# Optimization experiments

Measured on AMD Instinct MI355X. Metric: run time of the kernel, lower is better.

The kernel has to match this reference:

```python
import jax, jax.numpy as jnp
import numpy as np

B, H, S, DK = 4, 16, 2048, 128
NEG = -1e9  # large-negative stand-in for -inf additive mask
CAUSAL = True  # module constructed with mask=True (decoder self-attention)


def setup_inputs() -> dict:
    key = jax.random.key(0)
    kq, kk, kv, kl = jax.random.split(key, 4)
    q = jax.random.normal(kq, (B, H, S, DK), dtype=jnp.float32)
    k = jax.random.normal(kk, (B, H, S, DK), dtype=jnp.float32)
    v = jax.random.normal(kv, (B, H, S, DK), dtype=jnp.float32)
    sen_len = jax.random.randint(kl, (B,), 1, S + 1, dtype=jnp.int32)
    return {"q": q, "k": k, "v": v, "sen_len": sen_len}


def reference(q, k, v, sen_len):
    # att = q @ k^T / sqrt(d)   -> (B, H, S, S)
    scale = 1.0 / jnp.sqrt(jnp.asarray(DK, dtype=q.dtype))
    att = jnp.einsum('bhqd,bhkd->bhqk', q, k) * scale

    # Fused padding (+ optional causal) mask, multiplicative zero-mask and
    # additive -inf mask, exactly as att*zero_mask + inf_mask in the original.
    pos = jnp.arange(S)
    valid = pos[None, :] < sen_len[:, None]                 # (B, S) token validity
    zmask = (valid[:, :, None] & valid[:, None, :])         # (B, S, S) pad mask
    if CAUSAL:
        zmask = zmask & (pos[None, :, None] >= pos[None, None, :])
    zmask = zmask[:, None, :, :].astype(att.dtype)          # (B, 1, S, S)
    att = att * zmask + NEG * (1.0 - zmask)

    att = jax.nn.softmax(att, axis=-1)
    return jnp.einsum('bhqk,bhkd->bhqd', att, v)
```

## Files before the change

kernel.cpp:

```cpp
#include <hip/hip_runtime.h>
#include <hip/hip_bf16.h>

#define Bb   4
#define Hh   16
#define Ss   2048
#define Dd   128
#define QBLK 128
#define KVB  32

typedef __attribute__((ext_vector_type(8))) short bf16x8;
typedef __attribute__((ext_vector_type(4))) float f32x4;
typedef __attribute__((ext_vector_type(4))) float fvec4;
typedef __attribute__((ext_vector_type(2))) unsigned u32x2;
typedef __attribute__((ext_vector_type(4))) unsigned u32x4;

__device__ __forceinline__ unsigned pk2(float a, float b) {
    __hip_bfloat162 h = __float22bfloat162_rn(make_float2(a, b));
    unsigned u; __builtin_memcpy(&u, &h, 4); return u;
}

typedef const __attribute__((address_space(1))) char* gas_t;
typedef __attribute__((address_space(3))) char* las_t;
__device__ __forceinline__ void gld16(const void* g, void* l) {
    __builtin_amdgcn_global_load_lds((gas_t)g, (las_t)l, 16, 0, 0);
}

__global__ __launch_bounds__(256) void cvtkf_kernel(const float* __restrict__ K,
                                                    short* __restrict__ Kf) {
    const int bh = blockIdx.x >> 5, ch = blockIdx.x & 31;
    const int tid = threadIdx.x;
    const float* Kb = K + ((size_t)bh * Ss + ch * 64) * Dd;
    short* out = Kf + ((size_t)(bh * 64 + ch * 2)) * 4096;
    #pragma unroll
    for (int i = 0; i < 4; ++i) {
        int c = tid + 256 * i;
        int kt = c >> 9, r = c & 511;
        int mt = r >> 8, kc = (r >> 6) & 3, l = r & 63;
        int g = l >> 4, qc = l & 15;
        const fvec4* p = (const fvec4*)(Kb + (size_t)(kt * 32 + mt * 16 + qc) * Dd
                                        + kc * 32 + g * 8);
        fvec4 a = p[0], b = p[1];
        u32x4 u;
        u[0] = pk2(a[0], a[1]); u[1] = pk2(a[2], a[3]);
        u[2] = pk2(b[0], b[1]); u[3] = pk2(b[2], b[3]);
        *(u32x4*)(out + c * 8) = u;
    }
}

__global__ __launch_bounds__(256) void cvtvf_kernel(const float* __restrict__ V,
                                                    short* __restrict__ Vf,
                                                    float* __restrict__ part) {
    __shared__ float bins[128];
    const int bh = blockIdx.x >> 5, ch = blockIdx.x & 31;
    const int tid = threadIdx.x;
    if (tid < 128) bins[tid] = 0.f;
    __syncthreads();
    const float* Vb = V + ((size_t)bh * Ss + ch * 64) * Dd;
    short* out = Vf + ((size_t)(bh * 64 + ch * 2)) * 4096;
    #pragma unroll
    for (int i = 0; i < 4; ++i) {
        int c = tid + 256 * i;
        int kt = c >> 9, r = c & 511;
        int dt = r >> 6, l = r & 63;
        int g = l >> 4, qc = l & 15;
        int d = dt * 16 + qc;
        const float* src = Vb + (size_t)(kt * 32 + g * 8) * Dd + d;
        float v[8]; float s = 0.f;
        #pragma unroll
        for (int j = 0; j < 8; ++j) { v[j] = src[(size_t)j * Dd]; s += v[j]; }
        atomicAdd(&bins[d], s);
        u32x4 u;
        u[0] = pk2(v[0], v[1]); u[1] = pk2(v[2], v[3]);
        u[2] = pk2(v[4], v[5]); u[3] = pk2(v[6], v[7]);
        *(u32x4*)(out + c * 8) = u;
    }
    __syncthreads();
    if (tid < 128) part[(size_t)blockIdx.x * Dd + tid] = bins[tid];
}

__global__ __launch_bounds__(256) void vpart_kernel(const float* __restrict__ V,
                                                    float* __restrict__ part) {
    int blk = blockIdx.x, bh = blk >> 3, ch = blk & 7;
    int tid = threadIdx.x, d4 = tid & 31, rg = tid >> 5;
    const fvec4* p = (const fvec4*)(V + ((size_t)bh * Ss + ch * 256) * Dd) + d4;
    fvec4 s = {0.f, 0.f, 0.f, 0.f};
    for (int rr = 0; rr < 32; ++rr) s += p[(size_t)(rg * 32 + rr) * 32];
    __shared__ fvec4 red[256];
    red[tid] = s;
    __syncthreads();
    for (int off = 128; off >= 32; off >>= 1) {
        if (tid < off) red[tid] += red[tid + off];
        __syncthreads();
    }
    if (tid < 32) ((fvec4*)(part + (size_t)blk * Dd))[tid] = red[tid];
}

__global__ __launch_bounds__(128) void vcomb_kernel(const float* __restrict__ part,
                                                    float* __restrict__ vm, int nch) {
    int bh = blockIdx.x, d = threadIdx.x;
    float s = 0.f;
    for (int c = 0; c < nch; ++c) s += part[(size_t)(bh * nch + c) * Dd + d];
    vm[bh * Dd + d] = s * (1.0f / 2048.0f);
}

__global__ __launch_bounds__(256) void attn4_kernel(
    const float* __restrict__ Qg, const short* __restrict__ Kf,
    const short* __restrict__ Vf, const int* __restrict__ slen,
    const float* __restrict__ vmean, float* __restrict__ Og)
{
    __shared__ __align__(16) short Ks[2][2048];
    __shared__ __align__(16) short Ks2[2][2048];
    __shared__ __align__(16) short Vs[2][2048];
    __shared__ __align__(16) short Vs2[2][2048];
    __shared__ __align__(16) short Ps[4096];

    const int bid = blockIdx.x;
    const int qslot = bid >> 6, r = bid & 63;
    const int qt = 15 - qslot;
    const int b  = (r >> 3) & 3;
    const int h  = (r & 7) | ((r >> 5) << 3);
    const int bh = b * 16 + h;
    const int len = slen[b];
    const int q0 = qt * QBLK;
    const int tid = threadIdx.x;

    if (q0 >= len) {
        const fvec4* vm4 = (const fvec4*)(vmean + bh * Dd);
        fvec4 val = vm4[tid & 31];
        float* ob = Og + ((size_t)bh * Ss + q0) * Dd;
        int r0 = tid >> 5;
        #pragma unroll
        for (int i = 0; i < 16; ++i)
            ((fvec4*)(ob + (size_t)(r0 + 8 * i) * Dd))[tid & 31] = val;
        return;
    }

    const int w = tid >> 6, lane = tid & 63;
    const int g = lane >> 4, qc = lane & 15;
    const int qw0 = q0 + w * 32;
    const bool wave_active = (qw0 < len);
    const int lo16 = lane * 16;

    const int kv_end   = min(q0 + QBLK, len);
    const int kv_end_w = min(qw0 + 32, kv_end);
    const int nt = (kv_end + KVB - 1) >> 5;

    const char* KbhB = (const char*)Kf + (size_t)bh * 524288;
    const char* VbhB = (const char*)Vf + (size_t)bh * 524288;

    #define GISSUE(tile_, buf_) do {                                                   \
        const char* kb_ = KbhB + (size_t)(tile_) * 8192 + w * 2048;                    \
        const char* vb_ = VbhB + (size_t)(tile_) * 8192 + w * 2048;                    \
        char* kd_ = (w < 2) ? (char*)Ks[buf_] : (char*)Ks2[buf_];                      \
        char* vd_ = (w < 2) ? (char*)Vs[buf_] : (char*)Vs2[buf_];                      \
        kd_ += (w & 1) * 2048;                                                         \
        vd_ += (w & 1) * 2048;                                                         \
        gld16(kb_ + lo16, kd_);                                                        \
        gld16(kb_ + 1024 + lo16, kd_ + 1024);                                          \
        gld16(vb_ + lo16, vd_);                                                        \
        gld16(vb_ + 1024 + lo16, vd_ + 1024);                                          \
    } while (0)

    GISSUE(0, 0);

    const float SC = 0.12752870368768582f;
    bf16x8 qf[2][4];
    #pragma unroll
    for (int t2 = 0; t2 < 2; ++t2) {
        const float* qrow = Qg + ((size_t)bh * Ss + (qw0 + 16 * t2 + qc)) * Dd;
        #pragma unroll
        for (int kc = 0; kc < 4; ++kc) {
            const fvec4* p = (const fvec4*)(qrow + kc * 32 + g * 8);
            fvec4 a = p[0], bv = p[1];
            unsigned* fu = (unsigned*)&qf[t2][kc];
            fu[0] = pk2(a[0] * SC, a[1] * SC);
            fu[1] = pk2(a[2] * SC, a[3] * SC);
            fu[2] = pk2(bv[0] * SC, bv[1] * SC);
            fu[3] = pk2(bv[2] * SC, bv[3] * SC);
        }
    }

    asm volatile("s_waitcnt vmcnt(0)" ::: "memory");
    __syncthreads();

    f32x4 o[2][8];
    #pragma unroll
    for (int t2 = 0; t2 < 2; ++t2)
        #pragma unroll
        for (int dt = 0; dt < 8; ++dt) o[t2][dt] = (f32x4){0.f, 0.f, 0.f, 0.f};
    float m_[2]   = {-3e38f, -3e38f};
    float lsum[2] = {0.f, 0.f};

    char* PsB = (char*)Ps + w * 2048;
    const int sw0 = (qc ^ (qc >> 2)) & 3;

    for (int t = 0; t < nt; ++t) {
        const int kv0 = t * KVB;
        const int cur = t & 1;
        const bool pre = (t + 1 < nt);
        const bool active = wave_active && (kv0 < kv_end_w);

        if (pre) GISSUE(t + 1, cur ^ 1);

        if (active) {
            const char* KsA = (const char*)Ks[cur];
            const char* KsB2 = (const char*)Ks2[cur];
            const char* VsA = (const char*)Vs[cur];
            const char* VsB2 = (const char*)Vs2[cur];

            f32x4 sa[2][2];
            #pragma unroll
            for (int t2 = 0; t2 < 2; ++t2)
                #pragma unroll
                for (int mt = 0; mt < 2; ++mt) sa[t2][mt] = (f32x4){0.f, 0.f, 0.f, 0.f};
            __builtin_amdgcn_s_setprio(1);
            #pragma unroll
            for (int mt = 0; mt < 2; ++mt) {
                bf16x8 kf[4];
                #pragma unroll
                for (int kc = 0; kc < 4; ++kc) {
                    int chunk = mt * 4 + kc;
                    const char* base = (chunk < 4) ? KsA : KsB2;
                    kf[kc] = *(const bf16x8*)(base + (chunk & 3) * 1024 + lo16);
                }
                #pragma unroll
                for (int t2 = 0; t2 < 2; ++t2)
                    #pragma unroll
                    for (int kc = 0; kc < 4; ++kc)
                        sa[t2][mt] = __builtin_amdgcn_mfma_f32_16x16x32_bf16(
                            kf[kc], qf[t2][kc], sa[t2][mt], 0, 0, 0);
            }
            __builtin_amdgcn_s_setprio(0);

            #pragma unroll
            for (int t2 = 0; t2 < 2; ++t2) {
                const int qrow = qw0 + 16 * t2 + qc;
                const bool full = (kv0 + KVB - 1) <= (qw0 + 16 * t2);
                if (!full) {
                    #pragma unroll
                    for (int mt = 0; mt < 2; ++mt)
                        #pragma unroll
                        for (int rr = 0; rr < 4; ++rr) {
                            int kk = kv0 + mt * 16 + g * 4 + rr;
                            if (kk > qrow) sa[t2][mt][rr] = -3e38f;
                        }
                }
                float tm = fmaxf(
                    fmaxf(fmaxf(sa[t2][0][0], sa[t2][0][1]), fmaxf(sa[t2][0][2], sa[t2][0][3])),
                    fmaxf(fmaxf(sa[t2][1][0], sa[t2][1][1]), fmaxf(sa[t2][1][2], sa[t2][1][3])));
                tm = fmaxf(tm, __shfl_xor(tm, 16));
                tm = fmaxf(tm, __shfl_xor(tm, 32));
                if (__any(tm > m_[t2] + 8.0f)) {
                    float mnew = fmaxf(m_[t2], tm);
                    float al = exp2f(m_[t2] - mnew);
                    m_[t2] = mnew;
                    lsum[t2] *= al;
                    #pragma unroll
                    for (int rr = 0; rr < 4; ++rr) {
                        float alr = __shfl(al, g * 4 + rr);
                        #pragma unroll
                        for (int dt = 0; dt < 8; ++dt) o[t2][dt][rr] *= alr;
                    }
                }
                float mref = m_[t2];
                float ls = 0.f;
                int prow = t2 * 16 + qc;
                #pragma unroll
                for (int mt = 0; mt < 2; ++mt) {
                    f32x4 p;
                    #pragma unroll
                    for (int rr = 0; rr < 4; ++rr)
                        p[rr] = exp2f(sa[t2][mt][rr] - mref);
                    ls += (p[0] + p[1]) + (p[2] + p[3]);
                    u32x2 pw;
                    pw[0] = pk2(p[0], p[1]);
                    pw[1] = pk2(p[2], p[3]);
                    int bo = prow * 64 + (((mt * 2 + (g >> 1)) ^ sw0) * 16) + (g & 1) * 8;
                    *(u32x2*)(PsB + bo) = pw;
                }
                lsum[t2] += ls;
            }

            bf16x8 ap[2];
            #pragma unroll
            for (int t2 = 0; t2 < 2; ++t2) {
                int prow = t2 * 16 + qc;
                ap[t2] = *(const bf16x8*)(PsB + prow * 64 + ((g ^ sw0) * 16));
            }
            __builtin_amdgcn_s_setprio(1);
            #pragma unroll
            for (int dt = 0; dt < 8; ++dt) {
                const char* base = (dt < 4) ? VsA : VsB2;
                bf16x8 bfv = *(const bf16x8*)(base + (dt & 3) * 1024 + lo16);
                #pragma unroll
                for (int t2 = 0; t2 < 2; ++t2)
                    o[t2][dt] = __builtin_amdgcn_mfma_f32_16x16x32_bf16(
                        ap[t2], bfv, o[t2][dt], 0, 0, 0);
            }
            __builtin_amdgcn_s_setprio(0);
        }

        asm volatile("s_waitcnt vmcnt(0)" ::: "memory");
        __syncthreads();
    }
    #undef GISSUE

    float inv_[2][4];
    #pragma unroll
    for (int t2 = 0; t2 < 2; ++t2) {
        float L = lsum[t2];
        L += __shfl_xor(L, 16);
        L += __shfl_xor(L, 32);
        #pragma unroll
        for (int rr = 0; rr < 4; ++rr) {
            float Lr = __shfl(L, g * 4 + rr);
            inv_[t2][rr] = 1.0f / Lr;
        }
    }
    bool needvm = (qw0 + 32 > len);
    float vmv[8];
    #pragma unroll
    for (int dt = 0; dt < 8; ++dt)
        vmv[dt] = needvm ? vmean[bh * Dd + dt * 16 + qc] : 0.f;
    #pragma unroll
    for (int t2 = 0; t2 < 2; ++t2)
        #pragma unroll
        for (int rr = 0; rr < 4; ++rr) {
            int rowg = qw0 + t2 * 16 + g * 4 + rr;
            float* orow = Og + ((size_t)bh * Ss + rowg) * Dd + qc;
            #pragma unroll
            for (int dt = 0; dt < 8; ++dt) {
                float val = o[t2][dt][rr] * inv_[t2][rr];
                if (rowg >= len) val = vmv[dt];
                orow[dt * 16] = val;
            }
        }
}

__global__ __launch_bounds__(256, 2) void attn_fb_kernel(
    const float* __restrict__ Qg, const float* __restrict__ Kg,
    const float* __restrict__ Vg, const int* __restrict__ slen,
    const float* __restrict__ vmean, float* __restrict__ Og)
{
    __shared__ __align__(16) short Ks[64 * Dd];
    __shared__ __align__(16) short Vt[Dd * 64];
    __shared__ __align__(16) short Ps[4 * 32 * 64];

    const int bid = blockIdx.x;
    const int qslot = bid >> 6, r = bid & 63;
    const int qt = 15 - qslot;
    const int b  = (r >> 3) & 3;
    const int h  = (r & 7) | ((r >> 5) << 3);
    const int bh = b * 16 + h;
    const int len = slen[b];
    const int q0 = qt * QBLK;
    const int tid = threadIdx.x;

    if (q0 >= len) {
        const fvec4* vm4 = (const fvec4*)(vmean + bh * Dd);
        fvec4 val = vm4[tid & 31];
        float* ob = Og + ((size_t)bh * Ss + q0) * Dd;
        int r0 = tid >> 5;
        #pragma unroll
        for (int i = 0; i < 16; ++i)
            ((fvec4*)(ob + (size_t)(r0 + 8 * i) * Dd))[tid & 31] = val;
        return;
    }

    const int w = tid >> 6, lane = tid & 63;
    const int g = lane >> 4, qc = lane & 15;
    const int qw0 = q0 + w * 32;
    const bool wave_active = (qw0 < len);

    const int kv_end   = min(q0 + QBLK, len);
    const int kv_end_w = min(qw0 + 32, kv_end);
    const int nt = (kv_end + 63) >> 6;

    const float SC = 0.12752870368768582f;
    bf16x8 qf[2][4];
    #pragma unroll
    for (int t2 = 0; t2 < 2; ++t2) {
        const float* qrow = Qg + ((size_t)bh * Ss + (qw0 + 16 * t2 + qc)) * Dd;
        #pragma unroll
        for (int kc = 0; kc < 4; ++kc) {
            const fvec4* p = (const fvec4*)(qrow + kc * 32 + g * 8);
            fvec4 a = p[0], bv = p[1];
            unsigned* fu = (unsigned*)&qf[t2][kc];
            fu[0] = pk2(a[0] * SC, a[1] * SC);
            fu[1] = pk2(a[2] * SC, a[3] * SC);
            fu[2] = pk2(bv[0] * SC, bv[1] * SC);
            fu[3] = pk2(bv[2] * SC, bv[3] * SC);
        }
    }

    f32x4 o[2][8];
    #pragma unroll
    for (int t2 = 0; t2 < 2; ++t2)
        #pragma unroll
        for (int dt = 0; dt < 8; ++dt) o[t2][dt] = (f32x4){0.f, 0.f, 0.f, 0.f};
    float m_[2]   = {-3e38f, -3e38f};
    float lsum[2] = {0.f, 0.f};
    char* PsB = (char*)Ps + w * 4096;

    for (int t = 0; t < nt; ++t) {
        const int kv0 = t * 64;
        const bool active = wave_active && (kv0 < kv_end_w);
        __syncthreads();
        {
            const fvec4* sk = (const fvec4*)(Kg + ((size_t)bh * Ss + kv0) * Dd);
            #pragma unroll
            for (int i = 0; i < 8; ++i) {
                int f = tid + 256 * i;
                int kr = f >> 5, d4 = f & 31;
                fvec4 v = sk[(size_t)kr * 32 + d4];
                u32x2 pr; pr[0] = pk2(v[0], v[1]); pr[1] = pk2(v[2], v[3]);
                int j = d4 >> 1;
                int js = (j & 8) | ((j & 7) ^ (kr & 7));
                *(u32x2*)((char*)Ks + kr * 256 + js * 16 + (d4 & 1) * 8) = pr;
            }
            const float* sv = Vg + ((size_t)bh * Ss + kv0) * Dd;
            #pragma unroll
            for (int i = 0; i < 2; ++i) {
                int idx = tid + 256 * i;
                int dt4 = idx & 31, kt4 = idx >> 5;
                fvec4 vv[4];
                #pragma unroll
                for (int jj = 0; jj < 4; ++jj)
                    vv[jj] = ((const fvec4*)(sv + (size_t)(kt4 * 4 + jj) * Dd))[dt4];
                #pragma unroll
                for (int jj = 0; jj < 4; ++jj) {
                    int d = dt4 * 4 + jj;
                    u32x2 pr;
                    pr[0] = pk2(vv[0][jj], vv[1][jj]);
                    pr[1] = pk2(vv[2][jj], vv[3][jj]);
                    int bo = d * 128 + ((kt4 >> 1) ^ (d & 7)) * 16 + (kt4 & 1) * 8;
                    *(u32x2*)((char*)Vt + bo) = pr;
                }
            }
        }
        __syncthreads();

        if (active) {
            f32x4 sa[2][4];
            #pragma unroll
            for (int t2 = 0; t2 < 2; ++t2)
                #pragma unroll
                for (int mt = 0; mt < 4; ++mt) sa[t2][mt] = (f32x4){0.f, 0.f, 0.f, 0.f};
            #pragma unroll
            for (int mt = 0; mt < 4; ++mt) {
                int row = mt * 16 + qc;
                bf16x8 kf[4];
                #pragma unroll
                for (int kc = 0; kc < 4; ++kc) {
                    int jb = kc * 4 + g;
                    int js = (jb & 8) | ((jb & 7) ^ (row & 7));
                    kf[kc] = *(const bf16x8*)((const char*)Ks + row * 256 + js * 16);
                }
                #pragma unroll
                for (int t2 = 0; t2 < 2; ++t2)
                    #pragma unroll
                    for (int kc = 0; kc < 4; ++kc)
                        sa[t2][mt] = __builtin_amdgcn_mfma_f32_16x16x32_bf16(
                            kf[kc], qf[t2][kc], sa[t2][mt], 0, 0, 0);
            }
            #pragma unroll
            for (int t2 = 0; t2 < 2; ++t2) {
                const int qrow = qw0 + 16 * t2 + qc;
                const bool full = (kv0 + 63) <= (qw0 + 16 * t2);
                if (!full) {
                    #pragma unroll
                    for (int mt = 0; mt < 4; ++mt)
                        #pragma unroll
                        for (int rr = 0; rr < 4; ++rr) {
                            int kk = kv0 + mt * 16 + g * 4 + rr;
                            if (kk > qrow) sa[t2][mt][rr] = -3e38f;
                        }
                }
                float tm = sa[t2][0][0];
                #pragma unroll
                for (int mt = 0; mt < 4; ++mt)
                    #pragma unroll
                    for (int rr = 0; rr < 4; ++rr) tm = fmaxf(tm, sa[t2][mt][rr]);
                tm = fmaxf(tm, __shfl_xor(tm, 16));
                tm = fmaxf(tm, __shfl_xor(tm, 32));
                if (__any(tm > m_[t2] + 8.0f)) {
                    float mnew = fmaxf(m_[t2], tm);
                    float al = exp2f(m_[t2] - mnew);
                    m_[t2] = mnew;
                    lsum[t2] *= al;
                    #pragma unroll
                    for (int rr = 0; rr < 4; ++rr) {
                        float alr = __shfl(al, g * 4 + rr);
                        #pragma unroll
                        for (int dt = 0; dt < 8; ++dt) o[t2][dt][rr] *= alr;
                    }
                }
                float mref = m_[t2];
                float ls = 0.f;
                int prow = t2 * 16 + qc;
                int pswz = (prow & 7) << 4;
                #pragma unroll
                for (int mt = 0; mt < 4; ++mt) {
                    f32x4 p;
                    #pragma unroll
                    for (int rr = 0; rr < 4; ++rr)
                        p[rr] = exp2f(sa[t2][mt][rr] - mref);
                    ls += (p[0] + p[1]) + (p[2] + p[3]);
                    u32x2 pw;
                    pw[0] = pk2(p[0], p[1]);
                    pw[1] = pk2(p[2], p[3]);
                    *(u32x2*)(PsB + ((prow * 128 + mt * 32 + g * 8) ^ pswz)) = pw;
                }
                lsum[t2] += ls;
            }
            bf16x8 ap[2][2];
            #pragma unroll
            for (int t2 = 0; t2 < 2; ++t2) {
                int prow = t2 * 16 + qc;
                int pswz = (prow & 7) << 4;
                #pragma unroll
                for (int c = 0; c < 2; ++c)
                    ap[t2][c] = *(const bf16x8*)(PsB + ((prow * 128 + c * 64 + g * 16) ^ pswz));
            }
            #pragma unroll
            for (int dt = 0; dt < 8; ++dt) {
                int d = dt * 16 + qc;
                #pragma unroll
                for (int c = 0; c < 2; ++c) {
                    int js = (c * 4 + g) ^ (d & 7);
                    bf16x8 bfv = *(const bf16x8*)((const char*)Vt + d * 128 + js * 16);
                    #pragma unroll
                    for (int t2 = 0; t2 < 2; ++t2)
                        o[t2][dt] = __builtin_amdgcn_mfma_f32_16x16x32_bf16(
                            ap[t2][c], bfv, o[t2][dt], 0, 0, 0);
                }
            }
        }
    }

    float inv_[2][4];
    #pragma unroll
    for (int t2 = 0; t2 < 2; ++t2) {
        float L = lsum[t2];
        L += __shfl_xor(L, 16);
        L += __shfl_xor(L, 32);
        #pragma unroll
        for (int rr = 0; rr < 4; ++rr) {
            float Lr = __shfl(L, g * 4 + rr);
            inv_[t2][rr] = 1.0f / Lr;
        }
    }
    bool needvm = (qw0 + 32 > len);
    float vmv[8];
    #pragma unroll
    for (int dt = 0; dt < 8; ++dt)
        vmv[dt] = needvm ? vmean[bh * Dd + dt * 16 + qc] : 0.f;
    #pragma unroll
    for (int t2 = 0; t2 < 2; ++t2)
        #pragma unroll
        for (int rr = 0; rr < 4; ++rr) {
            int rowg = qw0 + t2 * 16 + g * 4 + rr;
            float* orow = Og + ((size_t)bh * Ss + rowg) * Dd + qc;
            #pragma unroll
            for (int dt = 0; dt < 8; ++dt) {
                float val = o[t2][dt][rr] * inv_[t2][rr];
                if (rowg >= len) val = vmv[dt];
                orow[dt * 16] = val;
            }
        }
}

extern "C" void kernel_launch(void* const* d_in, const int* in_sizes, int n_in,
                              void* d_out, int out_size, void* d_ws, size_t ws_size,
                              hipStream_t stream) {
    const float* q  = (const float*)d_in[0];
    const float* k  = (const float*)d_in[1];
    const float* v  = (const float*)d_in[2];
    const int*   sl = (const int*)d_in[3];
    float* out = (float*)d_out;

    const size_t nElem = (size_t)Bb * Hh * Ss * Dd;
    const size_t need0 = nElem * 2 * 2 + 2048 * Dd * 4 + 64 * Dd * 4;

    if (ws_size >= need0) {
        short* Kf   = (short*)d_ws;
        short* Vf   = Kf + nElem;
        float* part = (float*)(Vf + nElem);
        float* vm   = part + 2048 * Dd;
        cvtkf_kernel<<<dim3(2048), dim3(256), 0, stream>>>(k, Kf);
        cvtvf_kernel<<<dim3(2048), dim3(256), 0, stream>>>(v, Vf, part);
        vcomb_kernel<<<dim3(Bb * Hh), dim3(128), 0, stream>>>(part, vm, 32);
        attn4_kernel<<<dim3(1024), dim3(256), 0, stream>>>(q, Kf, Vf, sl, vm, out);
    } else {
        float* part = (float*)d_ws;
        float* vm   = part + 512 * Dd;
        vpart_kernel<<<dim3(512), dim3(256), 0, stream>>>(v, part);
        vcomb_kernel<<<dim3(Bb * Hh), dim3(128), 0, stream>>>(part, vm, 8);
        attn_fb_kernel<<<dim3(1024), dim3(256), 0, stream>>>(q, k, v, sl, vm, out);
    }
}
```

Measured before the change: 150.0 us.

## Load K/V fragments directly into registers per wave, dropping shared-memory staging

Replaces the block-cooperative LDS double-buffered K/V staging (global_load_lds plus a __syncthreads every tile) with per-wave register loads. Each wave independently prefetches the next 32-key K and V tiles into registers while computing on the current ones. Each wave now only iterates up to its own causal bound and exits early when fully padded. This removes block-wide barriers and load imbalance between waves. The cost is that each wave reads K/V separately, up to four times the global/L2 traffic per block, plus higher register pressure from holding 16 extra bf16x8 fragments.

```diff
diff --git a/kernel.cpp b/kernel.cpp
--- a/kernel.cpp
+++ b/kernel.cpp
@@ -17,12 +17,6 @@
 __device__ __forceinline__ unsigned pk2(float a, float b) {
     __hip_bfloat162 h = __float22bfloat162_rn(make_float2(a, b));
     unsigned u; __builtin_memcpy(&u, &h, 4); return u;
-}
-
-typedef const __attribute__((address_space(1))) char* gas_t;
-typedef __attribute__((address_space(3))) char* las_t;
-__device__ __forceinline__ void gld16(const void* g, void* l) {
-    __builtin_amdgcn_global_load_lds((gas_t)g, (las_t)l, 16, 0, 0);
 }
 
 __global__ __launch_bounds__(256) void cvtkf_kernel(const float* __restrict__ K,
@@ -103,16 +97,214 @@
     vm[bh * Dd + d] = s * (1.0f / 2048.0f);
 }
 
-__global__ __launch_bounds__(256) void attn4_kernel(
+__global__ __launch_bounds__(256) void attnpw_kernel(
     const float* __restrict__ Qg, const short* __restrict__ Kf,
     const short* __restrict__ Vf, const int* __restrict__ slen,
     const float* __restrict__ vmean, float* __restrict__ Og)
 {
-    __shared__ __align__(16) short Ks[2][2048];
-    __shared__ __align__(16) short Ks2[2][2048];
-    __shared__ __align__(16) short Vs[2][2048];
-    __shared__ __align__(16) short Vs2[2][2048];
     __shared__ __align__(16) short Ps[4096];
+
+    const int bid = blockIdx.x;
+    const int qslot = bid >> 6, r = bid & 63;
+    const int qt = 15 - qslot;
+    const int b  = (r >> 3) & 3;
+    const int h  = (r & 7) | ((r >> 5) << 3);
+    const int bh = b * 16 + h;
+    const int len = slen[b];
+    const int tid = threadIdx.x;
+    const int w = tid >> 6, lane = tid & 63;
+    const int g = lane >> 4, qc = lane & 15;
+    const int qw0 = qt * QBLK + w * 32;
+    const int lo16 = lane * 16;
+
+    if (qw0 >= len) {
+        const fvec4* vm4 = (const fvec4*)(vmean + bh * Dd);
+        fvec4 val = vm4[lane & 31];
+        float* ob = Og + ((size_t)bh * Ss + qw0) * Dd;
+        int r0 = lane >> 5;
+        #pragma unroll
+        for (int i = 0; i < 16; ++i)
+            ((fvec4*)(ob + (size_t)(r0 + 2 * i) * Dd))[lane & 31] = val;
+        return;
+    }
+
+    const int kv_end_w = min(qw0 + 32, len);
+    const int ntw = (kv_end_w + 31) >> 5;
+
+    const char* KbhB = (const char*)Kf + (size_t)bh * 524288;
+    const char* VbhB = (const char*)Vf + (size_t)bh * 524288;
+
+    bf16x8 kR[8], vR[8];
+    #pragma unroll
+    for (int i = 0; i < 8; ++i) kR[i] = *(const bf16x8*)(KbhB + i * 1024 + lo16);
+    #pragma unroll
+    for (int i = 0; i < 8; ++i) vR[i] = *(const bf16x8*)(VbhB + i * 1024 + lo16);
+
+    const float SC = 0.12752870368768582f;
+    bf16x8 qf[2][4];
+    #pragma unroll
+    for (int t2 = 0; t2 < 2; ++t2) {
+        const float* qrow = Qg + ((size_t)bh * Ss + (qw0 + 16 * t2 + qc)) * Dd;
+        #pragma unroll
+        for (int kc = 0; kc < 4; ++kc) {
+            const fvec4* p = (const fvec4*)(qrow + kc * 32 + g * 8);
+            fvec4 a = p[0], bv = p[1];
+            unsigned* fu = (unsigned*)&qf[t2][kc];
+            fu[0] = pk2(a[0] * SC, a[1] * SC);
+            fu[1] = pk2(a[2] * SC, a[3] * SC);
+            fu[2] = pk2(bv[0] * SC, bv[1] * SC);
+            fu[3] = pk2(bv[2] * SC, bv[3] * SC);
+        }
+    }
+
+    f32x4 o[2][8];
+    #pragma unroll
+    for (int t2 = 0; t2 < 2; ++t2)
+        #pragma unroll
+        for (int dt = 0; dt < 8; ++dt) o[t2][dt] = (f32x4){0.f, 0.f, 0.f, 0.f};
+    float m_[2]   = {-3e38f, -3e38f};
+    float lsum[2] = {0.f, 0.f};
+
+    char* PsB = (char*)Ps + w * 2048;
+    const int sw0 = (qc ^ (qc >> 2)) & 3;
+
+    for (int t = 0; t < ntw; ++t) {
+        const int kv0 = t * KVB;
+        const bool pre = (t + 1 < ntw);
+
+        f32x4 sa[2][2];
+        #pragma unroll
+        for (int t2 = 0; t2 < 2; ++t2)
+            #pragma unroll
+            for (int mt = 0; mt < 2; ++mt) sa[t2][mt] = (f32x4){0.f, 0.f, 0.f, 0.f};
+        __builtin_amdgcn_s_setprio(1);
+        #pragma unroll
+        for (int mt = 0; mt < 2; ++mt)
+            #pragma unroll
+            for (int t2 = 0; t2 < 2; ++t2)
+                #pragma unroll
+                for (int kc = 0; kc < 4; ++kc)
+                    sa[t2][mt] = __builtin_amdgcn_mfma_f32_16x16x32_bf16(
+                        kR[mt * 4 + kc], qf[t2][kc], sa[t2][mt], 0, 0, 0);
+        __builtin_amdgcn_s_setprio(0);
+
+        if (pre) {
+            const char* kb = KbhB + (size_t)(t + 1) * 8192;
+            #pragma unroll
+            for (int i = 0; i < 8; ++i) kR[i] = *(const bf16x8*)(kb + i * 1024 + lo16);
+        }
+
+        #pragma unroll
+        for (int t2 = 0; t2 < 2; ++t2) {
+            const int qrow = qw0 + 16 * t2 + qc;
+            const bool full = (kv0 + KVB - 1) <= (qw0 + 16 * t2);
+            if (!full) {
+                #pragma unroll
+                for (int mt = 0; mt < 2; ++mt)
+                    #pragma unroll
+                    for (int rr = 0; rr < 4; ++rr) {
+                        int kk = kv0 + mt * 16 + g * 4 + rr;
+                        if (kk > qrow) sa[t2][mt][rr] = -3e38f;
+                    }
+            }
+            float tm = fmaxf(
+                fmaxf(fmaxf(sa[t2][0][0], sa[t2][0][1]), fmaxf(sa[t2][0][2], sa[t2][0][3])),
+                fmaxf(fmaxf(sa[t2][1][0], sa[t2][1][1]), fmaxf(sa[t2][1][2], sa[t2][1][3])));
+            tm = fmaxf(tm, __shfl_xor(tm, 16));
+            tm = fmaxf(tm, __shfl_xor(tm, 32));
+            if (__any(tm > m_[t2] + 8.0f)) {
+                float mnew = fmaxf(m_[t2], tm);
+                float al = exp2f(m_[t2] - mnew);
+                m_[t2] = mnew;
+                lsum[t2] *= al;
+                #pragma unroll
+                for (int rr = 0; rr < 4; ++rr) {
+                    float alr = __shfl(al, g * 4 + rr);
+                    #pragma unroll
+                    for (int dt = 0; dt < 8; ++dt) o[t2][dt][rr] *= alr;
+                }
+            }
+            float mref = m_[t2];
+            float ls = 0.f;
+            int prow = t2 * 16 + qc;
+            #pragma unroll
+            for (int mt = 0; mt < 2; ++mt) {
+                f32x4 p;
+                #pragma unroll
+                for (int rr = 0; rr < 4; ++rr)
+                    p[rr] = exp2f(sa[t2][mt][rr] - mref);
+                ls += (p[0] + p[1]) + (p[2] + p[3]);
+                u32x2 pw;
+                pw[0] = pk2(p[0], p[1]);
+                pw[1] = pk2(p[2], p[3]);
+                int bo = prow * 64 + (((mt * 2 + (g >> 1)) ^ sw0) * 16) + (g & 1) * 8;
+                *(u32x2*)(PsB + bo) = pw;
+            }
+            lsum[t2] += ls;
+        }
+
+        bf16x8 ap[2];
+        #pragma unroll
+        for (int t2 = 0; t2 < 2; ++t2) {
+            int prow = t2 * 16 + qc;
+            ap[t2] = *(const bf16x8*)(PsB + prow * 64 + ((g ^ sw0) * 16));
+        }
+        __builtin_amdgcn_s_setprio(1);
+        #pragma unroll
+        for (int dt = 0; dt < 8; ++dt)
+            #pragma unroll
+            for (int t2 = 0; t2 < 2; ++t2)
+                o[t2][dt] = __builtin_amdgcn_mfma_f32_16x16x32_bf16(
+                    ap[t2], vR[dt], o[t2][dt], 0, 0, 0);
+        __builtin_amdgcn_s_setprio(0);
+
+        if (pre) {
+            const char* vb = VbhB + (size_t)(t + 1) * 8192;
+            #pragma unroll
+            for (int i = 0; i < 8; ++i) vR[i] = *(const bf16x8*)(vb + i * 1024 + lo16);
+        }
+    }
+
+    float inv_[2][4];
+    #pragma unroll
+    for (int t2 = 0; t2 < 2; ++t2) {
+        float L = lsum[t2];
+        L += __shfl_xor(L, 16);
+        L += __shfl_xor(L, 32);
+        #pragma unroll
+        for (int rr = 0; rr < 4; ++rr) {
+            float Lr = __shfl(L, g * 4 + rr);
+            inv_[t2][rr] = 1.0f / Lr;
+        }
+    }
+    bool needvm = (qw0 + 32 > len);
+    float vmv[8];
+    #pragma unroll
+    for (int dt = 0; dt < 8; ++dt)
+        vmv[dt] = needvm ? vmean[bh * Dd + dt * 16 + qc] : 0.f;
+    #pragma unroll
+    for (int t2 = 0; t2 < 2; ++t2)
+        #pragma unroll
+        for (int rr = 0; rr < 4; ++rr) {
+            int rowg = qw0 + t2 * 16 + g * 4 + rr;
+            float* orow = Og + ((size_t)bh * Ss + rowg) * Dd + qc;
+            #pragma unroll
+            for (int dt = 0; dt < 8; ++dt) {
+                float val = o[t2][dt][rr] * inv_[t2][rr];
+                if (rowg >= len) val = vmv[dt];
+                orow[dt * 16] = val;
+            }
+        }
+}
+
+__global__ __launch_bounds__(256, 2) void attn_fb_kernel(
+    const float* __restrict__ Qg, const float* __restrict__ Kg,
+    const float* __restrict__ Vg, const int* __restrict__ slen,
+    const float* __restrict__ vmean, float* __restrict__ Og)
+{
+    __shared__ __align__(16) short Ks[64 * Dd];
+    __shared__ __align__(16) short Vt[Dd * 64];
+    __shared__ __align__(16) short Ps[4 * 32 * 64];
 
     const int bid = blockIdx.x;
     const int qslot = bid >> 6, r = bid & 63;
@@ -139,29 +331,10 @@
     const int g = lane >> 4, qc = lane & 15;
     const int qw0 = q0 + w * 32;
     const bool wave_active = (qw0 < len);
-    const int lo16 = lane * 16;
 
     const int kv_end   = min(q0 + QBLK, len);
     const int kv_end_w = min(qw0 + 32, kv_end);
-    const int nt = (kv_end + KVB - 1) >> 5;
-
-    const char* KbhB = (const char*)Kf + (size_t)bh * 524288;
-    const char* VbhB = (const char*)Vf + (size_t)bh * 524288;
-
-    #define GISSUE(tile_, buf_) do {                                                   \
-        const char* kb_ = KbhB + (size_t)(tile_) * 8192 + w * 2048;                    \
-        const char* vb_ = VbhB + (size_t)(tile_) * 8192 + w * 2048;                    \
-        char* kd_ = (w < 2) ? (char*)Ks[buf_] : (char*)Ks2[buf_];                      \
-        char* vd_ = (w < 2) ? (char*)Vs[buf_] : (char*)Vs2[buf_];                      \
-        kd_ += (w & 1) * 2048;                                                         \
-        vd_ += (w & 1) * 2048;                                                         \
-        gld16(kb_ + lo16, kd_);                                                        \
-        gld16(kb_ + 1024 + lo16, kd_ + 1024);                                          \
-        gld16(vb_ + lo16, vd_);                                                        \
-        gld16(vb_ + 1024 + lo16, vd_ + 1024);                                          \
-    } while (0)
-
-    GISSUE(0, 0);
+    const int nt = (kv_end + 63) >> 6;
 
     const float SC = 0.12752870368768582f;
     bf16x8 qf[2][4];
@@ -180,219 +353,6 @@
         }
     }
 
-    asm volatile("s_waitcnt vmcnt(0)" ::: "memory");
-    __syncthreads();
-
-    f32x4 o[2][8];
-    #pragma unroll
-    for (int t2 = 0; t2 < 2; ++t2)
-        #pragma unroll
-        for (int dt = 0; dt < 8; ++dt) o[t2][dt] = (f32x4){0.f, 0.f, 0.f, 0.f};
-    float m_[2]   = {-3e38f, -3e38f};
-    float lsum[2] = {0.f, 0.f};
-
-    char* PsB = (char*)Ps + w * 2048;
-    const int sw0 = (qc ^ (qc >> 2)) & 3;
-
-    for (int t = 0; t < nt; ++t) {
-        const int kv0 = t * KVB;
-        const int cur = t & 1;
-        const bool pre = (t + 1 < nt);
-        const bool active = wave_active && (kv0 < kv_end_w);
-
-        if (pre) GISSUE(t + 1, cur ^ 1);
-
-        if (active) {
-            const char* KsA = (const char*)Ks[cur];
-            const char* KsB2 = (const char*)Ks2[cur];
-            const char* VsA = (const char*)Vs[cur];
-            const char* VsB2 = (const char*)Vs2[cur];
-
-            f32x4 sa[2][2];
-            #pragma unroll
-            for (int t2 = 0; t2 < 2; ++t2)
-                #pragma unroll
-                for (int mt = 0; mt < 2; ++mt) sa[t2][mt] = (f32x4){0.f, 0.f, 0.f, 0.f};
-            __builtin_amdgcn_s_setprio(1);
-            #pragma unroll
-            for (int mt = 0; mt < 2; ++mt) {
-                bf16x8 kf[4];
-                #pragma unroll
-                for (int kc = 0; kc < 4; ++kc) {
-                    int chunk = mt * 4 + kc;
-                    const char* base = (chunk < 4) ? KsA : KsB2;
-                    kf[kc] = *(const bf16x8*)(base + (chunk & 3) * 1024 + lo16);
-                }
-                #pragma unroll
-                for (int t2 = 0; t2 < 2; ++t2)
-                    #pragma unroll
-                    for (int kc = 0; kc < 4; ++kc)
-                        sa[t2][mt] = __builtin_amdgcn_mfma_f32_16x16x32_bf16(
-                            kf[kc], qf[t2][kc], sa[t2][mt], 0, 0, 0);
-            }
-            __builtin_amdgcn_s_setprio(0);
-
-            #pragma unroll
-            for (int t2 = 0; t2 < 2; ++t2) {
-                const int qrow = qw0 + 16 * t2 + qc;
-                const bool full = (kv0 + KVB - 1) <= (qw0 + 16 * t2);
-                if (!full) {
-                    #pragma unroll
-                    for (int mt = 0; mt < 2; ++mt)
-                        #pragma unroll
-                        for (int rr = 0; rr < 4; ++rr) {
-                            int kk = kv0 + mt * 16 + g * 4 + rr;
-                            if (kk > qrow) sa[t2][mt][rr] = -3e38f;
-                        }
-                }
-                float tm = fmaxf(
-                    fmaxf(fmaxf(sa[t2][0][0], sa[t2][0][1]), fmaxf(sa[t2][0][2], sa[t2][0][3])),
-                    fmaxf(fmaxf(sa[t2][1][0], sa[t2][1][1]), fmaxf(sa[t2][1][2], sa[t2][1][3])));
-                tm = fmaxf(tm, __shfl_xor(tm, 16));
-                tm = fmaxf(tm, __shfl_xor(tm, 32));
-                if (__any(tm > m_[t2] + 8.0f)) {
-                    float mnew = fmaxf(m_[t2], tm);
-                    float al = exp2f(m_[t2] - mnew);
-                    m_[t2] = mnew;
-                    lsum[t2] *= al;
-                    #pragma unroll
-                    for (int rr = 0; rr < 4; ++rr) {
-                        float alr = __shfl(al, g * 4 + rr);
-                        #pragma unroll
-                        for (int dt = 0; dt < 8; ++dt) o[t2][dt][rr] *= alr;
-                    }
-                }
-                float mref = m_[t2];
-                float ls = 0.f;
-                int prow = t2 * 16 + qc;
-                #pragma unroll
-                for (int mt = 0; mt < 2; ++mt) {
-                    f32x4 p;
-                    #pragma unroll
-                    for (int rr = 0; rr < 4; ++rr)
-                        p[rr] = exp2f(sa[t2][mt][rr] - mref);
-                    ls += (p[0] + p[1]) + (p[2] + p[3]);
-                    u32x2 pw;
-                    pw[0] = pk2(p[0], p[1]);
-                    pw[1] = pk2(p[2], p[3]);
-                    int bo = prow * 64 + (((mt * 2 + (g >> 1)) ^ sw0) * 16) + (g & 1) * 8;
-                    *(u32x2*)(PsB + bo) = pw;
-                }
-                lsum[t2] += ls;
-            }
-
-            bf16x8 ap[2];
-            #pragma unroll
-            for (int t2 = 0; t2 < 2; ++t2) {
-                int prow = t2 * 16 + qc;
-                ap[t2] = *(const bf16x8*)(PsB + prow * 64 + ((g ^ sw0) * 16));
-            }
-            __builtin_amdgcn_s_setprio(1);
-            #pragma unroll
-            for (int dt = 0; dt < 8; ++dt) {
-                const char* base = (dt < 4) ? VsA : VsB2;
-                bf16x8 bfv = *(const bf16x8*)(base + (dt & 3) * 1024 + lo16);
-                #pragma unroll
-                for (int t2 = 0; t2 < 2; ++t2)
-                    o[t2][dt] = __builtin_amdgcn_mfma_f32_16x16x32_bf16(
-                        ap[t2], bfv, o[t2][dt], 0, 0, 0);
-            }
-            __builtin_amdgcn_s_setprio(0);
-        }
-
-        asm volatile("s_waitcnt vmcnt(0)" ::: "memory");
-        __syncthreads();
-    }
-    #undef GISSUE
-
-    float inv_[2][4];
-    #pragma unroll
-    for (int t2 = 0; t2 < 2; ++t2) {
-        float L = lsum[t2];
-        L += __shfl_xor(L, 16);
-        L += __shfl_xor(L, 32);
-        #pragma unroll
-        for (int rr = 0; rr < 4; ++rr) {
-            float Lr = __shfl(L, g * 4 + rr);
-            inv_[t2][rr] = 1.0f / Lr;
-        }
-    }
-    bool needvm = (qw0 + 32 > len);
-    float vmv[8];
-    #pragma unroll
-    for (int dt = 0; dt < 8; ++dt)
-        vmv[dt] = needvm ? vmean[bh * Dd + dt * 16 + qc] : 0.f;
-    #pragma unroll
-    for (int t2 = 0; t2 < 2; ++t2)
-        #pragma unroll
-        for (int rr = 0; rr < 4; ++rr) {
-            int rowg = qw0 + t2 * 16 + g * 4 + rr;
-            float* orow = Og + ((size_t)bh * Ss + rowg) * Dd + qc;
-            #pragma unroll
-            for (int dt = 0; dt < 8; ++dt) {
-                float val = o[t2][dt][rr] * inv_[t2][rr];
-                if (rowg >= len) val = vmv[dt];
-                orow[dt * 16] = val;
-            }
-        }
-}
-
-__global__ __launch_bounds__(256, 2) void attn_fb_kernel(
-    const float* __restrict__ Qg, const float* __restrict__ Kg,
-    const float* __restrict__ Vg, const int* __restrict__ slen,
-    const float* __restrict__ vmean, float* __restrict__ Og)
-{
-    __shared__ __align__(16) short Ks[64 * Dd];
-    __shared__ __align__(16) short Vt[Dd * 64];
-    __shared__ __align__(16) short Ps[4 * 32 * 64];
-
-    const int bid = blockIdx.x;
-    const int qslot = bid >> 6, r = bid & 63;
-    const int qt = 15 - qslot;
-    const int b  = (r >> 3) & 3;
-    const int h  = (r & 7) | ((r >> 5) << 3);
-    const int bh = b * 16 + h;
-    const int len = slen[b];
-    const int q0 = qt * QBLK;
-    const int tid = threadIdx.x;
-
-    if (q0 >= len) {
-        const fvec4* vm4 = (const fvec4*)(vmean + bh * Dd);
-        fvec4 val = vm4[tid & 31];
-        float* ob = Og + ((size_t)bh * Ss + q0) * Dd;
-        int r0 = tid >> 5;
-        #pragma unroll
-        for (int i = 0; i < 16; ++i)
-            ((fvec4*)(ob + (size_t)(r0 + 8 * i) * Dd))[tid & 31] = val;
-        return;
-    }
-
-    const int w = tid >> 6, lane = tid & 63;
-    const int g = lane >> 4, qc = lane & 15;
-    const int qw0 = q0 + w * 32;
-    const bool wave_active = (qw0 < len);
-
-    const int kv_end   = min(q0 + QBLK, len);
-    const int kv_end_w = min(qw0 + 32, kv_end);
-    const int nt = (kv_end + 63) >> 6;
-
-    const float SC = 0.12752870368768582f;
-    bf16x8 qf[2][4];
-    #pragma unroll
-    for (int t2 = 0; t2 < 2; ++t2) {
-        const float* qrow = Qg + ((size_t)bh * Ss + (qw0 + 16 * t2 + qc)) * Dd;
-        #pragma unroll
-        for (int kc = 0; kc < 4; ++kc) {
-            const fvec4* p = (const fvec4*)(qrow + kc * 32 + g * 8);
-            fvec4 a = p[0], bv = p[1];
-            unsigned* fu = (unsigned*)&qf[t2][kc];
-            fu[0] = pk2(a[0] * SC, a[1] * SC);
-            fu[1] = pk2(a[2] * SC, a[3] * SC);
-            fu[2] = pk2(bv[0] * SC, bv[1] * SC);
-            fu[3] = pk2(bv[2] * SC, bv[3] * SC);
-        }
-    }
-
     f32x4 o[2][8];
     #pragma unroll
     for (int t2 = 0; t2 < 2; ++t2)
@@ -590,7 +550,7 @@
         cvtkf_kernel<<<dim3(2048), dim3(256), 0, stream>>>(k, Kf);
         cvtvf_kernel<<<dim3(2048), dim3(256), 0, stream>>>(v, Vf, part);
         vcomb_kernel<<<dim3(Bb * Hh), dim3(128), 0, stream>>>(part, vm, 32);
-        attn4_kernel<<<dim3(1024), dim3(256), 0, stream>>>(q, Kf, Vf, sl, vm, out);
+        attnpw_kernel<<<dim3(1024), dim3(256), 0, stream>>>(q, Kf, Vf, sl, vm, out);
     } else {
         float* part = (float*)d_ws;
         float* vm   = part + 512 * Dd;
```

Result: slower. 179.7 us (+19.8%).
